# Optimization experiments

Measured on AMD Instinct MI355X. Metric: run time of the kernel, lower is better.

Reference implementation:

```python
import jax, jax.numpy as jnp
import numpy as np

# WAGE-style quantizer (NeuroSim training path): round to 2^(b-1) levels, clip to (-1+1/S, 1-1/S),
# straight-through estimator for gradients.

def wage_q(x, bits=8):
    S = 2.0 ** (bits - 1)
    q = jnp.clip(jnp.round(x * S) / S, -1.0 + 1.0 / S, 1.0 - 1.0 / S)
    return x + jax.lax.stop_gradient(q - x)


def qconv(x, w, stride, pad, wl_w=8, wl_a=8):
    wq = wage_q(w, wl_w)
    y = jax.lax.conv_general_dilated(
        x, wq, window_strides=(stride, stride),
        padding=[(pad, pad), (pad, pad)],
        dimension_numbers=('NCHW', 'OIHW', 'NCHW'))
    return wage_q(y, wl_a)


def pad_hw(x, p):
    return jnp.pad(x, ((0, 0), (0, 0), (p, p), (p, p)))


def crop_like(x, tgt):
    return x[:, :, :tgt.shape[2], :tgt.shape[3]]


WEIGHT_SHAPES = {
    'w1': (64, 4, 3, 3), 'w2': (128, 64, 3, 3), 'w3': (256, 128, 3, 3), 'w4': (512, 256, 3, 3),
    'wr11': (512, 512, 3, 3), 'wr12': (512, 512, 3, 3), 'wr21': (512, 512, 3, 3), 'wr22': (512, 512, 3, 3),
    'wd3': (128, 512, 4, 4), 'wd2': (64, 416, 4, 4), 'wd1': (4, 224, 4, 4),
    'wu43': (32, 512, 4, 4), 'wu32': (32, 416, 4, 4), 'wu21': (32, 224, 4, 4), 'wu10': (32, 100, 4, 4),
    'wfc': (1, 32),
}


def setup_inputs() -> dict:
    key = jax.random.key(0)
    keys = jax.random.split(key, len(WEIGHT_SHAPES) + 1)
    inp = {'x': jax.random.normal(keys[0], (8, 4, 256, 256), dtype=jnp.float32)}
    for i, (name, shp) in enumerate(WEIGHT_SHAPES.items()):
        fan_in = int(np.prod(shp[1:]))
        inp[name] = jax.random.normal(keys[i + 1], shp, dtype=jnp.float32) / np.sqrt(fan_in)
    return inp


def reference(x, w1, w2, w3, w4, wr11, wr12, wr21, wr22,
              wd3, wd2, wd1, wu43, wu32, wu21, wu10, wfc):
    c1 = qconv(x, w1, 2, 1)        # [B,64,128,128]
    c2 = qconv(c1, w2, 2, 1)       # [B,128,64,64]
    c3 = qconv(c2, w3, 2, 1)       # [B,256,32,32]
    c4 = qconv(c3, w4, 2, 1)       # [B,512,16,16]
    r11 = qconv(c4, wr11, 1, 1)
    r12 = (1.0 - qconv(r11, wr12, 1, 1)) * c4
    r21 = qconv(r12, wr21, 1, 1)
    r22 = (1.0 - qconv(r21, wr22, 1, 1)) * r12
    r22p = pad_hw(r22, 8)                                   # [B,512,32,32]
    flow4_up = crop_like(qconv(r22p, wu43, 1, 2), c3)       # [B,32,32,32]
    d3 = crop_like(qconv(r22p, wd3, 1, 2), c3)              # [B,128,32,32]
    cat3 = pad_hw(jnp.concatenate([c3, d3, flow4_up], 1), 16)  # [B,416,64,64]
    flow3_up = crop_like(qconv(cat3, wu32, 1, 2), c2)
    d2 = crop_like(qconv(cat3, wd2, 1, 2), c2)
    cat2 = pad_hw(jnp.concatenate([c2, d2, flow3_up], 1), 32)  # [B,224,128,128]
    flow2_up = crop_like(qconv(cat2, wu21, 1, 2), c1)
    d1 = crop_like(qconv(cat2, wd1, 1, 2), c1)
    cat1 = pad_hw(jnp.concatenate([c1, d1, flow2_up], 1), 64)  # [B,100,256,256]
    u10 = qconv(cat1, wu10, 1, 2)                              # [B,32,257,257]
    feat = jnp.max(u10, axis=(2, 3))                           # AdaptiveMaxPool2d((1,1))
    out = wage_q(feat @ wage_q(wfc, 8).T, 8)                   # QLinear 32->1
    return out
```

## Files before the change

kernel.cpp:

```cpp
#include <hip/hip_runtime.h>

#define DEV __device__ __forceinline__

typedef __attribute__((ext_vector_type(4))) int i32x4;

DEV int wqi(float y) {
    int q = (int)rintf(y * 128.0f);
    return q < -127 ? -127 : (q > 127 ? 127 : q);
}
DEV unsigned encf(float f) { unsigned u = __float_as_uint(f); return (u & 0x80000000u) ? ~u : (u | 0x80000000u); }
DEV float decf(unsigned u) { return (u & 0x80000000u) ? __uint_as_float(u ^ 0x80000000u) : __uint_as_float(~u); }
DEV float wq8f(float x) {
    float q = rintf(x * 128.0f) * 0.0078125f;
    return fminf(fmaxf(q, -0.9921875f), 0.9921875f);
}

#define GLOAD16(g, l) __builtin_amdgcn_global_load_lds( \
    (const __attribute__((address_space(1))) void*)(g), \
    (__attribute__((address_space(3))) void*)(l), 16, 0, 0)

struct PackDesc {
    const float* w0; const float* w1; uint4* dst;
    int OC0, OC1, CinW, K, noct, nch64u, ndup, gsz;
};
struct PackArgs { PackDesc d[11]; int bofs[12]; };

__global__ void __launch_bounds__(256) k_packall(PackArgs a) {
    __shared__ unsigned char sb[16 * (64 * 16 + 4)];
    const int b = blockIdx.x;
    int i = 0;
    #pragma unroll
    for (int j = 1; j < 11; ++j) if (b >= a.bofs[j]) i = j;
    const PackDesc D = a.d[i];
    const int b2 = b - a.bofs[i];
    const int oct = b2 % D.noct;
    const int ch64u = b2 / D.noct;
    const int K2 = D.K * D.K;
    const int NCHT = D.nch64u * D.ndup;
    const int row_elems = 64 * K2;
    const int SSTR = row_elems + 4;
    const int QR = row_elems / 4;
    const int NQ = 16 * QR;
    const int cin0 = ch64u * 64;
    const int tid = threadIdx.x;
    const int og = oct / D.gsz, ol = oct % D.gsz;

    for (int q = tid; q < NQ; q += 256) {
        const int r = q / QR, j = q - r * QR;
        const int oc = oct * 16 + r;
        const float* src = nullptr; int oci = 0;
        if (oc < D.OC0) { src = D.w0; oci = oc; }
        else if (oc < D.OC0 + D.OC1) { src = D.w1; oci = oc - D.OC0; }
        const int e0 = j * 4;
        float v[4] = {0.f, 0.f, 0.f, 0.f};
        if (src != nullptr) {
            const float* p = src + ((size_t)oci * D.CinW + cin0) * K2 + e0;
            const int cin_last = cin0 + (e0 + 3) / K2;
            if (cin_last < D.CinW) {
                const float4 f4 = *(const float4*)p;
                v[0] = f4.x; v[1] = f4.y; v[2] = f4.z; v[3] = f4.w;
            } else {
                #pragma unroll
                for (int e = 0; e < 4; ++e) {
                    const int cin = cin0 + (e0 + e) / K2;
                    if (cin < D.CinW) v[e] = p[e];
                }
            }
        }
        unsigned pk = 0;
        #pragma unroll
        for (int e = 0; e < 4; ++e) pk |= ((unsigned)(wqi(v[e]) & 255)) << (e * 8);
        *(unsigned*)&sb[r * SSTR + e0] = pk;
    }
    __syncthreads();

    const int outN = K2 * 64;
    for (int idx = tid; idx < outN; idx += 256) {
        const int kpos = idx >> 6, lane = idx & 63;
        const int l15 = lane & 15, g = lane >> 4;
        unsigned wd[4] = {0u, 0u, 0u, 0u};
        #pragma unroll
        for (int e = 0; e < 16; ++e) {
            const unsigned bval = sb[l15 * SSTR + (g * 16 + e) * K2 + kpos];
            wd[e >> 2] |= bval << ((e & 3) * 8);
        }
        uint4 u; u.x = wd[0]; u.y = wd[1]; u.z = wd[2]; u.w = wd[3];
        for (int d = 0; d < D.ndup; ++d) {
            const int ch64 = ch64u + d * D.nch64u;
            D.dst[((size_t)((og * NCHT + ch64) * K2 + kpos) * D.gsz + ol) * 64 + lane] = u;
        }
    }
}

__global__ void __launch_bounds__(256) k_zfill(uint4* __restrict__ p, int npix, int stride_u4,
                                               int off_u4, int cnt, int total) {
    const int idx = blockIdx.x * 256 + threadIdx.x;
    if (idx >= total) return;
    const int pix = idx / cnt, j = idx - pix * cnt;
    uint4 z; z.x = z.y = z.z = z.w = 0u;
    p[(size_t)pix * stride_u4 + off_u4 + j] = z;
}

__global__ void __launch_bounds__(256) k_conv1(const float* __restrict__ x, const float* __restrict__ w1,
                                               signed char* __restrict__ cat1) {
    __shared__ float sw2[36][64];
    __shared__ float sin_[4][17][17];
    const int tid = threadIdx.x;
    const int n = blockIdx.y;
    const int oh0 = (blockIdx.x >> 4) * 8, ow0 = (blockIdx.x & 15) * 8;
    for (int i = tid; i < 2304; i += 256) sw2[i % 36][i / 36] = wq8f(w1[i]);
    const int ih0 = oh0 * 2 - 1, iw0 = ow0 * 2 - 1;
    for (int i = tid; i < 4 * 289; i += 256) {
        const int c = i / 289, rem = i % 289, r = rem / 17, cc = rem % 17;
        const int ih = ih0 + r, iw = iw0 + cc;
        float v = 0.f;
        if ((unsigned)ih < 256u && (unsigned)iw < 256u) v = x[((size_t)(n * 4 + c) * 256 + ih) * 256 + iw];
        sin_[c][r][cc] = v;
    }
    __syncthreads();
    const int sp = tid & 63, ocg = tid >> 6;
    const int oh = sp >> 3, ow = sp & 7;
    float acc[16];
    #pragma unroll
    for (int j = 0; j < 16; ++j) acc[j] = 0.f;
    #pragma unroll
    for (int c = 0; c < 4; ++c)
    #pragma unroll
    for (int kh = 0; kh < 3; ++kh)
    #pragma unroll
    for (int kw = 0; kw < 3; ++kw) {
        const float v = sin_[c][oh * 2 + kh][ow * 2 + kw];
        const float4* wp4 = (const float4*)&sw2[c * 9 + kh * 3 + kw][ocg * 16];
        #pragma unroll
        for (int q = 0; q < 4; ++q) {
            const float4 wv = wp4[q];
            acc[q * 4 + 0] = fmaf(v, wv.x, acc[q * 4 + 0]);
            acc[q * 4 + 1] = fmaf(v, wv.y, acc[q * 4 + 1]);
            acc[q * 4 + 2] = fmaf(v, wv.z, acc[q * 4 + 2]);
            acc[q * 4 + 3] = fmaf(v, wv.w, acc[q * 4 + 3]);
        }
    }
    const size_t pix = ((size_t)(n * 128) + oh0 + oh) * 128 + ow0 + ow;
    unsigned wd[4] = {0u, 0u, 0u, 0u};
    #pragma unroll
    for (int j = 0; j < 16; ++j)
        wd[j >> 2] |= ((unsigned)(wqi(acc[j]) & 255)) << ((j & 3) * 8);
    uint4 u; u.x = wd[0]; u.y = wd[1]; u.z = wd[2]; u.w = wd[3];
    *(uint4*)(cat1 + pix * 112 + ocg * 16) = u;
}

__global__ void k_init(unsigned* __restrict__ feat, uint4* __restrict__ zbuf) {
    feat[threadIdx.x] = encf(0.0f);
    if (threadIdx.x < 64) { uint4 z; z.x = z.y = z.z = z.w = 0u; zbuf[threadIdx.x] = z; }
}

__global__ void k_fc(const unsigned* __restrict__ feat, const float* __restrict__ wfc,
                     float* __restrict__ out) {
    int n = threadIdx.x;
    if (n < 8) {
        float s = 0.f;
        for (int c = 0; c < 32; ++c) s += decf(feat[n * 32 + c]) * wq8f(wfc[c]);
        out[n] = wq8f(s);
    }
}

template<int CMODE>
__global__ void __launch_bounds__(256) k_comb(const int* __restrict__ ps, int D, int G,
                                              int NP, int OC, double inv,
                                              signed char* __restrict__ dst, int dstr, int dch,
                                              const void* __restrict__ res, int rstr,
                                              signed char* __restrict__ dhl, int dhlstr,
                                              short* __restrict__ dj,
                                              int ohw, int OWW, int r0, int r1, int c0, int c1) {
    const int t = blockIdx.x * 256 + threadIdx.x;
    const int opc = OC / 4;
    const int total = NP * opc;
    if (t >= total) return;
    const int pix = t / opc, oc0 = (t - pix * opc) * 4;
    const int sp = pix % ohw;
    const int oh = sp / OWW, ow = sp - oh * OWW;
    if (oh < r0 || oh > r1 || ow < c0 || ow > c1) return;
    const size_t base = (size_t)pix * OC + oc0;
    const size_t NPOC = (size_t)NP * OC;
    long v[4] = {0, 0, 0, 0};
    int sidx = 0;
    for (int d = 0; d < D; ++d) {
        long s0 = 0, s1 = 0, s2 = 0, s3 = 0;
        for (int g = 0; g < G; ++g, ++sidx) {
            const int4 p = *(const int4*)(ps + sidx * NPOC + base);
            s0 += p.x; s1 += p.y; s2 += p.z; s3 += p.w;
        }
        v[0] = v[0] * 256 + s0; v[1] = v[1] * 256 + s1;
        v[2] = v[2] * 256 + s2; v[3] = v[3] * 256 + s3;
    }
    if constexpr (CMODE == 0) {
        unsigned pk = 0;
        #pragma unroll
        for (int j = 0; j < 4; ++j)
            pk |= (unsigned)(wqi((float)((double)v[j] * inv)) & 255) << (j * 8);
        *(unsigned*)(dst + (size_t)pix * dstr + dch + oc0) = pk;
    } else {
        #pragma unroll
        for (int j = 0; j < 4; ++j) {
            const int qi = wqi((float)((double)v[j] * inv));
            const int oc = oc0 + j;
            if constexpr (CMODE == 1) {
                const int rv = (int)((const signed char*)res)[(size_t)pix * rstr + oc];
                const int jj = (128 - qi) * rv;
                const int d0 = ((jj + 128) & 255) - 128;
                const int t1 = (jj - d0) >> 8;
                dhl[(size_t)pix * dhlstr + oc] = (signed char)t1;
                dhl[(size_t)pix * dhlstr + 512 + oc] = (signed char)d0;
                dj[(size_t)pix * 512 + oc] = (short)jj;
            } else {
                const int rv = (int)((const short*)res)[(size_t)pix * rstr + oc];
                const int jj = (128 - qi) * rv;
                const int d0 = ((jj + 128) & 255) - 128;
                const int t1 = (jj - d0) >> 8;
                const int d1 = ((t1 + 128) & 255) - 128;
                const int d2 = (t1 - d1) >> 8;
                dhl[(size_t)pix * dhlstr + oc] = (signed char)d2;
                dhl[(size_t)pix * dhlstr + 512 + oc] = (signed char)d1;
                dhl[(size_t)pix * dhlstr + 1024 + oc] = (signed char)d0;
            }
        }
    }
}

template<int K, int STR, int WM, int WN, int BN, int CHQ, int NBUF, int MODE>
__global__ void __launch_bounds__(256) k_mconv(
    const signed char* __restrict__ s0, int Ctot, int st0,
    int S, int padeff,
    const uint4* __restrict__ wqp, int nchtot,
    signed char* __restrict__ dst, int dstr, int dch,
    unsigned* __restrict__ feat, int* __restrict__ ps,
    const signed char* __restrict__ zbuf,
    int OCv, int OH, int OW, int TILES_W, int nch,
    int NT, int NOCG, int swzq, int ORD, int ohb, int owb)
{
    constexpr int TH = WM * 4;
    constexpr int RH = (TH - 1) * STR + K, RW = 7 * STR + K;
    constexpr int UNITS = CHQ / 16;
    constexpr int UPPS = UNITS + 1;
    constexpr int NKC = CHQ / 64;
    constexpr int K2 = K * K;
    constexpr int NUS = RH * RW * UPPS;
    constexpr int ROUNDS = (NUS + 255) / 256;
    constexpr int NUPS = ROUNDS * 256;
    constexpr int AHEAD = NBUF - 1;
    __shared__ uint4 lds[NBUF * NUPS];
    __shared__ int sred[4][2][16];

    const int tid = threadIdx.x, lane = tid & 63, w = tid >> 6;
    const int wm = w % WM, wn = w / WM;
    const int l15 = lane & 15, g = lane >> 4;

    const int b = blockIdx.x;
    const int work = (b & 7) * swzq + (b >> 3);
    int tile, n, ocg, slice;
    if (ORD == 0) {
        ocg = work % NOCG; const int t2 = work / NOCG;
        tile = t2 % NT; const int t3 = t2 / NT;
        n = t3 & 7; slice = t3 >> 3;
    } else {
        tile = work % NT; const int t2 = work / NT;
        n = t2 & 7; const int t3 = t2 >> 3;
        ocg = t3 % NOCG; slice = t3 / NOCG;
    }
    const int cin_off = slice * nch * CHQ;
    const int group = ocg * WN + wn;

    const int tileh = tile / TILES_W, tilew = tile % TILES_W;
    const int oh0 = ohb + tileh * TH, ow0 = owb + tilew * 8;
    const int ih0 = oh0 * STR - padeff, iw0 = ow0 * STR - padeff;
    const int blk_oct0 = ocg * (WN * BN);

    int pixb[2];
    #pragma unroll
    for (int am = 0; am < 2; ++am) {
        const int sp = wm * 32 + am * 16 + l15;
        pixb[am] = ((sp >> 3) * STR) * RW + (sp & 7) * STR;
    }

    int climit[ROUNDS];
    const signed char* gpb[ROUNDS];
    #pragma unroll
    for (int rd = 0; rd < ROUNDS; ++rd) {
        const int d = rd * 256 + tid;
        int cl = -1;
        const signed char* gb = zbuf;
        if (d < NUS) {
            const int pix = d / UPPS;
            const int u = d - pix * UPPS;
            const int r = pix / RW, c = pix - r * RW;
            const int ih = ih0 + r, iw = iw0 + c;
            if (u < UNITS && (unsigned)ih < (unsigned)S && (unsigned)iw < (unsigned)S) {
                cl = Ctot - cin_off - u * 16;
                gb = s0 + (((size_t)n * S + ih) * S + iw) * st0 + cin_off + u * 16;
            }
        }
        climit[rd] = cl; gpb[rd] = gb;
    }

    i32x4 acc[2][BN];
    #pragma unroll
    for (int am = 0; am < 2; ++am)
        #pragma unroll
        for (int bn = 0; bn < BN; ++bn) acc[am][bn] = (i32x4){0, 0, 0, 0};

    auto issue = [&](int ch, int buf) {
        uint4* lb = &lds[buf * NUPS];
        const int chv = ch * CHQ;
        #pragma unroll
        for (int rd = 0; rd < ROUNDS; ++rd) {
            const signed char* gp = (chv < climit[rd]) ? (gpb[rd] + chv) : zbuf;
            GLOAD16(gp, lb + rd * 256 + (tid & ~63));
        }
    };

    #pragma unroll
    for (int i = 0; i < AHEAD; ++i) if (i < nch) issue(i, i % NBUF);

    for (int ch = 0; ch < nch; ++ch) {
        if (ch + AHEAD < nch) issue(ch + AHEAD, (ch + AHEAD) % NBUF);
        const int infl = (nch - 1 - ch < AHEAD) ? nch - 1 - ch : AHEAD;
        if (infl >= 2)      __builtin_amdgcn_s_waitcnt(0xF70 | (2 * ROUNDS));
        else if (infl == 1) __builtin_amdgcn_s_waitcnt(0xF70 | ROUNDS);
        else                __builtin_amdgcn_s_waitcnt(0xF70);
        __builtin_amdgcn_s_barrier();
        __builtin_amdgcn_sched_barrier(0);
        const int bufo = (ch % NBUF) * NUPS;
        const int pb0 = bufo + pixb[0] * UPPS + g;
        const int pb1 = bufo + pixb[1] * UPPS + g;
        const uint4* wrow = wqp + ((size_t)(group * nchtot + (slice * nch + ch) * NKC) * K2 * BN) * 64 + lane;
        #pragma unroll
        for (int kpos = 0; kpos < K2; ++kpos) {
            const int kh = kpos / K, kw = kpos % K;
            const int po = (kh * RW + kw) * UPPS;
            #pragma unroll
            for (int kc = 0; kc < NKC; ++kc) {
                i32x4 bfr[BN];
                #pragma unroll
                for (int bn = 0; bn < BN; ++bn) {
                    union { uint4 u; i32x4 v; } bu;
                    bu.u = wrow[(kc * K2 * BN + kpos * BN + bn) * 64];
                    bfr[bn] = bu.v;
                }
                union { uint4 u; i32x4 v; } a0, a1;
                a0.u = lds[pb0 + po + kc * 4];
                a1.u = lds[pb1 + po + kc * 4];
                #pragma unroll
                for (int bn = 0; bn < BN; ++bn) {
                    acc[0][bn] = __builtin_amdgcn_mfma_i32_16x16x64_i8(a0.v, bfr[bn], acc[0][bn], 0, 0, 0);
                    acc[1][bn] = __builtin_amdgcn_mfma_i32_16x16x64_i8(a1.v, bfr[bn], acc[1][bn], 0, 0, 0);
                }
            }
        }
        __builtin_amdgcn_sched_barrier(0);
        __builtin_amdgcn_s_barrier();
    }

    if constexpr (MODE == 2) {
        #pragma unroll
        for (int bn = 0; bn < BN; ++bn) {
            int m = (int)0x80000000;
            #pragma unroll
            for (int am = 0; am < 2; ++am)
                #pragma unroll
                for (int rg = 0; rg < 4; ++rg) {
                    const int sp = wm * 32 + am * 16 + g * 4 + rg;
                    const int oh = oh0 + (sp >> 3), ow = ow0 + (sp & 7);
                    const int v = acc[am][bn][rg];
                    if (oh < OH && ow < OW && v > m) m = v;
                }
            int o = __shfl_xor(m, 16); if (o > m) m = o;
            o = __shfl_xor(m, 32); if (o > m) m = o;
            if (lane < 16) sred[w][bn][l15] = m;
        }
        __syncthreads();
        if (tid < BN * 16) {
            const int bn = tid >> 4, l = tid & 15;
            int mm = sred[0][bn][l];
            #pragma unroll
            for (int i = 1; i < WM * WN; ++i) { const int o = sred[i][bn][l]; if (o > mm) mm = o; }
            const float y = (float)mm * (1.f / 16384.f);
            const float v = (float)wqi(y) * 0.0078125f;
            atomicMax(&feat[n * 32 + (blk_oct0 + bn) * 16 + l], encf(v));
        }
    } else if constexpr (MODE == 3) {
        #pragma unroll
        for (int am = 0; am < 2; ++am)
        #pragma unroll
        for (int bn = 0; bn < BN; ++bn)
        #pragma unroll
        for (int rg = 0; rg < 4; ++rg) {
            const int sp = wm * 32 + am * 16 + g * 4 + rg;
            const int oh = oh0 + (sp >> 3), ow = ow0 + (sp & 7);
            const int oc = (blk_oct0 + wn * BN + bn) * 16 + l15;
            if (oh < OH && ow < OW && oc < OCv) {
                ps[(((size_t)slice * 8 + n) * OH * OW + (size_t)oh * OW + ow) * OCv + oc] = acc[am][bn][rg];
            }
        }
    } else {
        #pragma unroll
        for (int am = 0; am < 2; ++am)
        #pragma unroll
        for (int bn = 0; bn < BN; ++bn)
        #pragma unroll
        for (int rg = 0; rg < 4; ++rg) {
            const int sp = wm * 32 + am * 16 + g * 4 + rg;
            const int oh = oh0 + (sp >> 3), ow = ow0 + (sp & 7);
            const int oc = (blk_oct0 + wn * BN + bn) * 16 + l15;
            if (oh < OH && ow < OW && oc < OCv) {
                const size_t pixo = (size_t)(n * OH + oh) * OW + ow;
                const float y = (float)acc[am][bn][rg] * (1.f / 16384.f);
                dst[pixo * dstr + dch + oc] = (signed char)wqi(y);
            }
        }
    }
}

extern "C" void kernel_launch(void* const* d_in, const int* in_sizes, int n_in,
                              void* d_out, int out_size, void* d_ws, size_t ws_size,
                              hipStream_t stream)
{
    (void)in_sizes; (void)n_in; (void)out_size; (void)ws_size;
    const float* x = (const float*)d_in[0];
    const float* wfc = (const float*)d_in[16];
    float* out = (float*)d_out;

    char* ws = (char*)d_ws;
    size_t off = 0;
    auto alloc = [&](size_t bytes) { char* p = ws + off; off += (bytes + 255) & ~(size_t)255; return p; };

    struct PH { int i0, OC0, i1, OC1, CinW, K, noct, nch64u, ndup, gsz; };
    static const PH ph[11] = {
        {2, 128, -1, 0,  64, 3,  8, 1, 1, 2},
        {3, 256, -1, 0, 128, 3, 16, 2, 1, 2},
        {4, 512, -1, 0, 256, 3, 32, 4, 1, 2},
        {5, 512, -1, 0, 512, 3, 32, 8, 1, 2},
        {6, 512, -1, 0, 512, 3, 32, 8, 1, 2},
        {7, 512, -1, 0, 512, 3, 32, 8, 2, 2},
        {8, 512, -1, 0, 512, 3, 32, 8, 1, 2},
        {9, 128, 12, 32, 512, 4, 10, 8, 3, 2},
        {10, 64, 13, 32, 416, 4,  6, 7, 1, 2},
        {11,  4, 14, 32, 224, 4,  3, 4, 1, 3},
        {15, 32, -1, 0, 100, 4,  2, 2, 1, 2}};

    PackArgs pa;
    int bacc = 0;
    uint4* wp[11];
    for (int i = 0; i < 11; ++i) {
        const int nch64 = ph[i].nch64u * ph[i].ndup;
        const int nel = nch64 * ph[i].K * ph[i].K * ph[i].noct * 64;
        wp[i] = (uint4*)alloc((size_t)nel * 16);
        pa.d[i].w0 = (const float*)d_in[ph[i].i0];
        pa.d[i].w1 = (ph[i].i1 >= 0) ? (const float*)d_in[ph[i].i1] : nullptr;
        pa.d[i].dst = wp[i];
        pa.d[i].OC0 = ph[i].OC0; pa.d[i].OC1 = ph[i].OC1;
        pa.d[i].CinW = ph[i].CinW; pa.d[i].K = ph[i].K; pa.d[i].noct = ph[i].noct;
        pa.d[i].nch64u = ph[i].nch64u; pa.d[i].ndup = ph[i].ndup;
        pa.d[i].gsz = ph[i].gsz;
        pa.bofs[i] = bacc;
        bacc += ph[i].noct * ph[i].nch64u;
    }
    pa.bofs[11] = bacc;

    signed char* cat1b = (signed char*)alloc((size_t)8*128*128*112);
    signed char* cat2b = (signed char*)alloc((size_t)8*64*64*224);
    signed char* cat3b = (signed char*)alloc((size_t)8*32*32*416);
    signed char* c4b   = (signed char*)alloc((size_t)8*16*16*512);
    signed char* r11b  = (signed char*)alloc((size_t)8*16*16*512);
    signed char* r12d  = (signed char*)alloc((size_t)8*16*16*1024);
    short*       r12j  = (short*)alloc((size_t)8*16*16*512 * 2);
    signed char* r22d  = (signed char*)alloc((size_t)8*16*16*1536);
    int*         psum  = (int*)alloc((size_t)4*8*16*16*512 * 4);
    unsigned*    featb = (unsigned*)alloc(256 * 4);
    uint4*       zbuf  = (uint4*)alloc(1024);

    k_packall<<<dim3((unsigned)bacc), dim3(256), 0, stream>>>(pa);
    k_init<<<dim3(1), dim3(256), 0, stream>>>(featb, zbuf);
    k_zfill<<<dim3((131072*3 + 255)/256), 256, 0, stream>>>((uint4*)cat1b, 131072, 7, 4, 3, 131072*3);
    k_zfill<<<dim3((32768*6 + 255)/256), 256, 0, stream>>>((uint4*)cat2b, 32768, 14, 8, 6, 32768*6);
    k_zfill<<<dim3((8192*10 + 255)/256), 256, 0, stream>>>((uint4*)cat3b, 8192, 26, 16, 10, 8192*10);
    k_conv1<<<dim3(256, 8), dim3(256), 0, stream>>>(x, (const float*)d_in[1], cat1b);

    const signed char* zb = (const signed char*)zbuf;
    const void* nv = nullptr;
    const int BIG = 1 << 30;

    k_mconv<3,2,2,2,2,64,1,0><<<dim3(1024), 256, 0, stream>>>(
        cat1b,64,112, 128,1, wp[0],1, cat2b,224,0, nullptr,nullptr, zb,
        128,64,64,8, 1, 64,2,128, 0, 0,0);
    k_mconv<3,2,2,2,2,64,2,0><<<dim3(512), 256, 0, stream>>>(
        cat2b,128,224, 64,1, wp[1],2, cat3b,416,0, nullptr,nullptr, zb,
        256,32,32,4, 2, 16,4,64, 0, 0,0);
    k_mconv<3,2,2,2,2,64,1,3><<<dim3(1024), 256, 0, stream>>>(
        cat3b,256,416, 32,1, wp[2],4, nullptr,0,0, nullptr,(int*)psum, zb,
        512,16,16,2, 1, 4,8,128, 1, 0,0);
    k_comb<0><<<dim3(1024), 256, 0, stream>>>(psum,1,4, 2048,512, 1.0/16384.0, c4b,512,0, nv,0, nullptr,0,nullptr,
        256,16, 0,BIG,0,BIG);
    k_mconv<3,1,4,1,2,128,1,3><<<dim3(1024), 256, 0, stream>>>(
        c4b,512,512, 16,1, wp[3],8, nullptr,0,0, nullptr,psum, zb,
        512,16,16,2, 1, 2,16,128, 1, 0,0);
    k_comb<0><<<dim3(1024), 256, 0, stream>>>(psum,1,4, 2048,512, 1.0/16384.0, r11b,512,0, nv,0, nullptr,0,nullptr,
        256,16, 0,BIG,0,BIG);
    k_mconv<3,1,4,1,2,64,3,3><<<dim3(512), 256, 0, stream>>>(
        r11b,512,512, 16,1, wp[4],8, nullptr,0,0, nullptr,psum, zb,
        512,16,16,2, 4, 2,16,64, 1, 0,0);
    k_comb<1><<<dim3(1024), 256, 0, stream>>>(psum,1,2, 2048,512, 1.0/16384.0, nullptr,0,0, c4b,512, r12d,1024,r12j,
        256,16, 0,BIG,0,BIG);
    k_mconv<3,1,4,1,2,64,2,3><<<dim3(1024), 256, 0, stream>>>(
        r12d,1024,1024, 16,1, wp[5],16, nullptr,0,0, nullptr,psum, zb,
        512,16,16,2, 4, 2,16,128, 1, 0,0);
    k_comb<0><<<dim3(1024), 256, 0, stream>>>(psum,2,2, 2048,512, 1.0/2097152.0, r11b,512,0, nv,0, nullptr,0,nullptr,
        256,16, 0,BIG,0,BIG);
    k_mconv<3,1,4,1,2,64,3,3><<<dim3(512), 256, 0, stream>>>(
        r11b,512,512, 16,1, wp[6],8, nullptr,0,0, nullptr,psum, zb,
        512,16,16,2, 4, 2,16,64, 1, 0,0);
    k_comb<2><<<dim3(1024), 256, 0, stream>>>(psum,1,2, 2048,512, 1.0/16384.0, nullptr,0,0, r12j,512, r22d,1536,nullptr,
        256,16, 0,BIG,0,BIG);
    k_mconv<4,1,4,1,2,64,2,3><<<dim3(720), 256, 0, stream>>>(
        r22d,1536,1536, 16,10, wp[7],24, nullptr,0,0, nullptr,psum, zb,
        160,32,32,3, 8, 6,5,90, 1, 7,7);
    k_comb<0><<<dim3(1280), 256, 0, stream>>>(psum,3,1, 8192,160, 1.0/268435456.0, cat3b,416,256, nv,0, nullptr,0,nullptr,
        1024,32, 7,25,7,25);
    k_mconv<4,1,4,1,2,64,2,0><<<dim3(360), 256, 0, stream>>>(
        cat3b,416,416, 32,18, wp[8],7, cat2b,224,128, nullptr,nullptr, zb,
        96,64,64,5, 7, 15,3,45, 0, 15,15);
    k_mconv<4,1,4,1,3,64,2,0><<<dim3(360), 256, 0, stream>>>(
        cat2b,224,224, 64,34, wp[9],4, cat1b,112,64, nullptr,nullptr, zb,
        48,128,128,9, 4, 45,1,45, 0, 31,31);
    k_mconv<4,1,4,1,2,128,1,2><<<dim3(1224), 256, 0, stream>>>(
        cat1b,112,112, 128,66, wp[10],2, nullptr,0,0, featb,nullptr, zb,
        32,257,257,17, 1, 153,1,153, 0, 63,63);
    k_fc<<<dim3(1), dim3(64), 0, stream>>>(featb, wfc, out);
}
```

Baseline: 298.1 us.

## Accumulate split-K partials with atomics and merge init/zero-fill kernels

Several split-K convolutions now atomically add their partial sums into one int buffer instead of writing separate slices, so the combine kernels read a single slice and zero that buffer after reading so the next layer can reuse it. The init and three zero-fill launches are merged into one prep kernel that also clears the partial-sum buffer. The decoder conv that keeps slice writes gets twice the K-split (more blocks, larger psum buffer). Atomics add contention and ordering nondeterminism, which is harmless here because the sums are integers, and the scheme depends on zeroing psum correctly between layers.

```diff
diff --git a/kernel.cpp b/kernel.cpp
--- a/kernel.cpp
+++ b/kernel.cpp
@@ -92,13 +92,39 @@
     }
 }
 
-__global__ void __launch_bounds__(256) k_zfill(uint4* __restrict__ p, int npix, int stride_u4,
-                                               int off_u4, int cnt, int total) {
-    const int idx = blockIdx.x * 256 + threadIdx.x;
-    if (idx >= total) return;
-    const int pix = idx / cnt, j = idx - pix * cnt;
+__global__ void __launch_bounds__(256) k_prep(unsigned* __restrict__ feat, uint4* __restrict__ zbuf,
+                                              uint4* __restrict__ ps0,
+                                              uint4* __restrict__ z1, uint4* __restrict__ z2,
+                                              uint4* __restrict__ z3) {
+    int b = blockIdx.x;
+    const int tid = threadIdx.x;
     uint4 z; z.x = z.y = z.z = z.w = 0u;
-    p[(size_t)pix * stride_u4 + off_u4 + j] = z;
+    if (b == 0) {
+        feat[tid] = encf(0.0f);
+        if (tid < 64) zbuf[tid] = z;
+        return;
+    }
+    b -= 1;
+    if (b < 1024) {
+        ps0[b * 256 + tid] = z; return;
+    }
+    b -= 1024;
+    if (b < 1536) {
+        const int i = b * 256 + tid;
+        if (i < 393216) { const int pix = i / 3, j = i - pix * 3; z1[(size_t)pix * 7 + 4 + j] = z; }
+        return;
+    }
+    b -= 1536;
+    if (b < 768) {
+        const int i = b * 256 + tid;
+        if (i < 196608) { const int pix = i / 6, j = i - pix * 6; z2[(size_t)pix * 14 + 8 + j] = z; }
+        return;
+    }
+    b -= 768;
+    {
+        const int i = b * 256 + tid;
+        if (i < 81920) { const int pix = i / 10, j = i - pix * 10; z3[(size_t)pix * 26 + 16 + j] = z; }
+    }
 }
 
 __global__ void __launch_bounds__(256) k_conv1(const float* __restrict__ x, const float* __restrict__ w1,
@@ -149,11 +175,6 @@
     *(uint4*)(cat1 + pix * 112 + ocg * 16) = u;
 }
 
-__global__ void k_init(unsigned* __restrict__ feat, uint4* __restrict__ zbuf) {
-    feat[threadIdx.x] = encf(0.0f);
-    if (threadIdx.x < 64) { uint4 z; z.x = z.y = z.z = z.w = 0u; zbuf[threadIdx.x] = z; }
-}
-
 __global__ void k_fc(const unsigned* __restrict__ feat, const float* __restrict__ wfc,
                      float* __restrict__ out) {
     int n = threadIdx.x;
@@ -171,7 +192,8 @@
                                               const void* __restrict__ res, int rstr,
                                               signed char* __restrict__ dhl, int dhlstr,
                                               short* __restrict__ dj,
-                                              int ohw, int OWW, int r0, int r1, int c0, int c1) {
+                                              int ohw, int OWW, int r0, int r1, int c0, int c1,
+                                              int* __restrict__ zp) {
     const int t = blockIdx.x * 256 + threadIdx.x;
     const int opc = OC / 4;
     const int total = NP * opc;
@@ -193,6 +215,7 @@
         v[0] = v[0] * 256 + s0; v[1] = v[1] * 256 + s1;
         v[2] = v[2] * 256 + s2; v[3] = v[3] * 256 + s3;
     }
+    if (zp) { int4 z; z.x = z.y = z.z = z.w = 0; *(int4*)(zp + base) = z; }
     if constexpr (CMODE == 0) {
         unsigned pk = 0;
         #pragma unroll
@@ -401,6 +424,20 @@
                 ps[(((size_t)slice * 8 + n) * OH * OW + (size_t)oh * OW + ow) * OCv + oc] = acc[am][bn][rg];
             }
         }
+    } else if constexpr (MODE == 4) {
+        #pragma unroll
+        for (int am = 0; am < 2; ++am)
+        #pragma unroll
+        for (int bn = 0; bn < BN; ++bn)
+        #pragma unroll
+        for (int rg = 0; rg < 4; ++rg) {
+            const int sp = wm * 32 + am * 16 + g * 4 + rg;
+            const int oh = oh0 + (sp >> 3), ow = ow0 + (sp & 7);
+            const int oc = (blk_oct0 + wn * BN + bn) * 16 + l15;
+            if (oh < OH && ow < OW && oc < OCv) {
+                atomicAdd(&ps[((size_t)n * OH * OW + (size_t)oh * OW + ow) * OCv + oc], acc[am][bn][rg]);
+            }
+        }
     } else {
         #pragma unroll
         for (int am = 0; am < 2; ++am)
@@ -474,15 +511,13 @@
     signed char* r12d  = (signed char*)alloc((size_t)8*16*16*1024);
     short*       r12j  = (short*)alloc((size_t)8*16*16*512 * 2);
     signed char* r22d  = (signed char*)alloc((size_t)8*16*16*1536);
-    int*         psum  = (int*)alloc((size_t)4*8*16*16*512 * 4);
+    int*         psum  = (int*)alloc((size_t)6*8*32*32*160 * 4);
     unsigned*    featb = (unsigned*)alloc(256 * 4);
     uint4*       zbuf  = (uint4*)alloc(1024);
 
     k_packall<<<dim3((unsigned)bacc), dim3(256), 0, stream>>>(pa);
-    k_init<<<dim3(1), dim3(256), 0, stream>>>(featb, zbuf);
-    k_zfill<<<dim3((131072*3 + 255)/256), 256, 0, stream>>>((uint4*)cat1b, 131072, 7, 4, 3, 131072*3);
-    k_zfill<<<dim3((32768*6 + 255)/256), 256, 0, stream>>>((uint4*)cat2b, 32768, 14, 8, 6, 32768*6);
-    k_zfill<<<dim3((8192*10 + 255)/256), 256, 0, stream>>>((uint4*)cat3b, 8192, 26, 16, 10, 8192*10);
+    k_prep<<<dim3(3649), 256, 0, stream>>>(featb, zbuf, (uint4*)psum,
+        (uint4*)cat1b, (uint4*)cat2b, (uint4*)cat3b);
     k_conv1<<<dim3(256, 8), dim3(256), 0, stream>>>(x, (const float*)d_in[1], cat1b);
 
     const signed char* zb = (const signed char*)zbuf;
@@ -495,36 +530,36 @@
     k_mconv<3,2,2,2,2,64,2,0><<<dim3(512), 256, 0, stream>>>(
         cat2b,128,224, 64,1, wp[1],2, cat3b,416,0, nullptr,nullptr, zb,
         256,32,32,4, 2, 16,4,64, 0, 0,0);
-    k_mconv<3,2,2,2,2,64,1,3><<<dim3(1024), 256, 0, stream>>>(
+    k_mconv<3,2,2,2,2,64,1,4><<<dim3(1024), 256, 0, stream>>>(
         cat3b,256,416, 32,1, wp[2],4, nullptr,0,0, nullptr,(int*)psum, zb,
         512,16,16,2, 1, 4,8,128, 1, 0,0);
-    k_comb<0><<<dim3(1024), 256, 0, stream>>>(psum,1,4, 2048,512, 1.0/16384.0, c4b,512,0, nv,0, nullptr,0,nullptr,
-        256,16, 0,BIG,0,BIG);
-    k_mconv<3,1,4,1,2,128,1,3><<<dim3(1024), 256, 0, stream>>>(
+    k_comb<0><<<dim3(1024), 256, 0, stream>>>(psum,1,1, 2048,512, 1.0/16384.0, c4b,512,0, nv,0, nullptr,0,nullptr,
+        256,16, 0,BIG,0,BIG, psum);
+    k_mconv<3,1,4,1,2,128,1,4><<<dim3(1024), 256, 0, stream>>>(
         c4b,512,512, 16,1, wp[3],8, nullptr,0,0, nullptr,psum, zb,
         512,16,16,2, 1, 2,16,128, 1, 0,0);
-    k_comb<0><<<dim3(1024), 256, 0, stream>>>(psum,1,4, 2048,512, 1.0/16384.0, r11b,512,0, nv,0, nullptr,0,nullptr,
-        256,16, 0,BIG,0,BIG);
-    k_mconv<3,1,4,1,2,64,3,3><<<dim3(512), 256, 0, stream>>>(
+    k_comb<0><<<dim3(1024), 256, 0, stream>>>(psum,1,1, 2048,512, 1.0/16384.0, r11b,512,0, nv,0, nullptr,0,nullptr,
+        256,16, 0,BIG,0,BIG, psum);
+    k_mconv<3,1,4,1,2,64,3,4><<<dim3(512), 256, 0, stream>>>(
         r11b,512,512, 16,1, wp[4],8, nullptr,0,0, nullptr,psum, zb,
         512,16,16,2, 4, 2,16,64, 1, 0,0);
-    k_comb<1><<<dim3(1024), 256, 0, stream>>>(psum,1,2, 2048,512, 1.0/16384.0, nullptr,0,0, c4b,512, r12d,1024,r12j,
-        256,16, 0,BIG,0,BIG);
+    k_comb<1><<<dim3(1024), 256, 0, stream>>>(psum,1,1, 2048,512, 1.0/16384.0, nullptr,0,0, c4b,512, r12d,1024,r12j,
+        256,16, 0,BIG,0,BIG, nullptr);
     k_mconv<3,1,4,1,2,64,2,3><<<dim3(1024), 256, 0, stream>>>(
         r12d,1024,1024, 16,1, wp[5],16, nullptr,0,0, nullptr,psum, zb,
         512,16,16,2, 4, 2,16,128, 1, 0,0);
     k_comb<0><<<dim3(1024), 256, 0, stream>>>(psum,2,2, 2048,512, 1.0/2097152.0, r11b,512,0, nv,0, nullptr,0,nullptr,
-        256,16, 0,BIG,0,BIG);
-    k_mconv<3,1,4,1,2,64,3,3><<<dim3(512), 256, 0, stream>>>(
+        256,16, 0,BIG,0,BIG, psum);
+    k_mconv<3,1,4,1,2,64,3,4><<<dim3(512), 256, 0, stream>>>(
         r11b,512,512, 16,1, wp[6],8, nullptr,0,0, nullptr,psum, zb,
         512,16,16,2, 4, 2,16,64, 1, 0,0);
-    k_comb<2><<<dim3(1024), 256, 0, stream>>>(psum,1,2, 2048,512, 1.0/16384.0, nullptr,0,0, r12j,512, r22d,1536,nullptr,
-        256,16, 0,BIG,0,BIG);
-    k_mconv<4,1,4,1,2,64,2,3><<<dim3(720), 256, 0, stream>>>(
+    k_comb<2><<<dim3(1024), 256, 0, stream>>>(psum,1,1, 2048,512, 1.0/16384.0, nullptr,0,0, r12j,512, r22d,1536,nullptr,
+        256,16, 0,BIG,0,BIG, nullptr);
+    k_mconv<4,1,4,1,2,64,2,3><<<dim3(1440), 256, 0, stream>>>(
         r22d,1536,1536, 16,10, wp[7],24, nullptr,0,0, nullptr,psum, zb,
-        160,32,32,3, 8, 6,5,90, 1, 7,7);
-    k_comb<0><<<dim3(1280), 256, 0, stream>>>(psum,3,1, 8192,160, 1.0/268435456.0, cat3b,416,256, nv,0, nullptr,0,nullptr,
-        1024,32, 7,25,7,25);
+        160,32,32,3, 4, 6,5,180, 1, 7,7);
+    k_comb<0><<<dim3(1280), 256, 0, stream>>>(psum,3,2, 8192,160, 1.0/268435456.0, cat3b,416,256, nv,0, nullptr,0,nullptr,
+        1024,32, 7,25,7,25, nullptr);
     k_mconv<4,1,4,1,2,64,2,0><<<dim3(360), 256, 0, stream>>>(
         cat3b,416,416, 32,18, wp[8],7, cat2b,224,128, nullptr,nullptr, zb,
         96,64,64,5, 7, 15,3,45, 0, 15,15);
```

Result: no change. 299.4 us (+0.4%).
